# Kernel optimization log

Measured on AMD Instinct MI355X. Metric: run time of the kernel, lower is better.

## Reference

```python
import jax, jax.numpy as jnp
import numpy as np
import math

B, N, CS, CZ = 1, 512, 384, 128
GD = 16            # ipa_conf.c_hidden -> num 3D groups G
CH = GD * 3        # per-head hidden = 48
H = 8
PQ, PV = 8, 12
NF = 4             # num_frequencies
INF, EPS = 1e5, 1e-8
CZ4 = CZ // 4


def base_frequencies(num_freqs=NF, base=8.0, max_freq=1.0):
    fs = [min(base ** (-2 * i / num_freqs) * max_freq, max_freq) for i in range(num_freqs)]
    return jnp.asarray(fs, dtype=jnp.float32)


def hat(v):
    # v: [..., 3] -> skew-symmetric [..., 3, 3]
    x, y, z = v[..., 0], v[..., 1], v[..., 2]
    o = jnp.zeros_like(x)
    return jnp.stack([
        jnp.stack([o, -z, y], -1),
        jnp.stack([z, o, -x], -1),
        jnp.stack([-y, x, o], -1)], -2)


def setup_inputs() -> dict:
    key = jax.random.key(0)
    ks = jax.random.split(key, 24)
    std = 0.02
    hc = CH * H
    hpkv = H * (PQ + PV) * 3
    inp = {
        's': jax.random.normal(ks[0], (B, N, CS), jnp.float32),
        'z': jax.random.normal(ks[1], (B, N, N, CZ), jnp.float32),
        'rotvec': jax.random.normal(ks[2], (B, N, 3), jnp.float32),
        'mask': jnp.ones((B, N), jnp.float32),
        'wq': jax.random.normal(ks[3], (CS, hc), jnp.float32) * std,
        'bq': jnp.zeros((hc,), jnp.float32),
        'wkv': jax.random.normal(ks[4], (CS, 2 * hc), jnp.float32) * std,
        'bkv': jnp.zeros((2 * hc,), jnp.float32),
        'wkvp': jax.random.normal(ks[5], (CS, hpkv), jnp.float32) * std,
        'bkvp': jnp.zeros((hpkv,), jnp.float32),
        'wb': jax.random.normal(ks[6], (CZ, H), jnp.float32) * std,
        'bb': jnp.zeros((H,), jnp.float32),
        'wdz': jax.random.normal(ks[7], (CZ, CZ4), jnp.float32) * std,
        'bdz': jnp.zeros((CZ4,), jnp.float32),
        'wout': jax.random.normal(ks[8], (H * (CZ4 + CH + PV * 4), CS), jnp.float32) * std,
        'bout': jnp.zeros((CS,), jnp.float32),
        'log_freq_adj': jax.random.normal(ks[9], (NF,), jnp.float32) * std,
        'group_weights': jax.random.normal(ks[10], (GD,), jnp.float32) * std,
        'freq_weights': jnp.full((NF,), 1.0 / NF, jnp.float32),
    }
    return inp


def reference(s, z, rotvec, mask, wq, bq, wkv, bkv, wkvp, bkvp, wb, bb,
              wdz, bdz, wout, bout, log_freq_adj, group_weights, freq_weights):
    G = GD
    # projections
    q = (s @ wq + bq).reshape(B, N, H, CH)
    kv = (s @ wkv + bkv).reshape(B, N, H, 2 * CH)
    k, v = kv[..., :CH], kv[..., CH:]
    P = PQ + PV
    kvp = (s @ wkvp + bkvp).reshape(B, N, 3, H * P)      # torch split(...,3)+stack(-1)
    kvp = jnp.moveaxis(kvp, -2, -1).reshape(B, N, H, P, 3)
    v_pts = kvp[..., PQ:, :]                             # [B,N,H,PV,3]
    bias = z @ wb + bb                                   # [B,N,N,H]
    # RoPE-inspired multi-frequency Rodrigues rotations
    nrm = jnp.linalg.norm(rotvec, axis=-1, keepdims=True)
    angle = nrm + 1e-8                                   # [B,N,1]
    axis = rotvec / jnp.maximum(nrm, 1e-12)
    freqs = base_frequencies() * jnp.exp(log_freq_adj)   # [F]
    theta = angle * freqs                                # [B,N,F]
    K = hat(axis)                                        # [B,N,3,3]
    K2 = K @ K
    sin_t = jnp.sin(theta)[..., None, None]              # [B,N,F,1,1]
    cos_t = jnp.cos(theta)[..., None, None]
    I3 = jnp.eye(3, dtype=s.dtype)
    R = I3 + sin_t * K[:, :, None] + (1.0 - cos_t) * K2[:, :, None]  # [B,N,F,3,3]
    qg = q.reshape(B, N, H, G, 3)
    kg = k.reshape(B, N, H, G, 3)
    q_rot = jnp.einsum('bnfij,bnhgj->bnhgfi', R, qg)     # [B,N,H,G,F,3]
    k_rot = jnp.einsum('bnfij,bnhgj->bnhgfi', R, kg)
    # aggregation weights (sum over groups, softmax-weighted freqs)
    freq_w = jax.nn.softmax(freq_weights)
    group_w = jax.nn.softplus(group_weights) * math.sqrt(1.0 / G)
    qw = q_rot * freq_w[None, None, None, None, :, None] * group_w[None, None, None, :, None, None]
    scores = jnp.einsum('bihgfc,bjhgfc->bhij', qw, k_rot) / math.sqrt(3.0)
    a = scores + math.sqrt(1.0 / 3.0) * jnp.transpose(bias, (0, 3, 1, 2))
    sq_mask = INF * (mask[:, :, None] * mask[:, None, :] - 1.0)
    a = jax.nn.softmax(a + sq_mask[:, None], axis=-1)    # [B,H,N,N]
    # outputs
    o = jnp.einsum('bhij,bjhc->bihc', a, v).reshape(B, N, H * CH)
    o_pt = jnp.einsum('bhij,bjhpc->bihpc', a, v_pts)     # [B,N,H,PV,3]
    o_pt_norm = jnp.sqrt(jnp.sum(o_pt ** 2, -1) + EPS).reshape(B, N, H * PV)
    o_pt_flat = o_pt.reshape(B, N, H * PV, 3)
    pair_z = z @ wdz + bdz                               # [B,N,N,CZ4]
    o_pair = jnp.einsum('bhij,bijc->bihc', a, pair_z).reshape(B, N, H * CZ4)
    feats = jnp.concatenate([o, o_pt_flat[..., 0], o_pt_flat[..., 1],
                             o_pt_flat[..., 2], o_pt_norm, o_pair], axis=-1)
    return feats @ wout + bout                           # [B,N,CS]
```

## Files before the change

### kernel.cpp

```cpp
#include <hip/hip_runtime.h>
#include <math.h>


#define OFF_PROJ 0
#define SZ_PROJ (512*1632)
#define OFF_QW (OFF_PROJ + SZ_PROJ)
#define SZ_QW (8*512*192)
#define OFF_KST (OFF_QW + SZ_QW)
#define OFF_VCAT (OFF_KST + SZ_QW)
#define SZ_VCAT (512*768)
#define OFF_A (OFF_VCAT + SZ_VCAT)
#define SZ_A (8*512*512)
#define OFF_FEATS (OFF_A + SZ_A)
#define SZ_FEATS (512*1024)
#define OFF_PART (OFF_FEATS + SZ_FEATS)
#define SZ_PART (8*512*384)

__global__ __launch_bounds__(256) void proj_kernel(
    const float* __restrict__ s, const float* __restrict__ wq, const float* __restrict__ bq,
    const float* __restrict__ wkv, const float* __restrict__ bkv,
    const float* __restrict__ wkvp, const float* __restrict__ bkvp,
    float* __restrict__ proj)
{
  __shared__ float sT[384][34];
  int ct = blockIdx.x;
  int i0 = blockIdx.y * 32;
  int col0 = ct * 64;
  const float* W; const float* bias; int wld, wcol0;
  if (col0 < 384)       { W = wq;   bias = bq;   wld = 384; wcol0 = col0; }
  else if (col0 < 1152) { W = wkv;  bias = bkv;  wld = 768; wcol0 = col0 - 384; }
  else                  { W = wkvp; bias = bkvp; wld = 480; wcol0 = col0 - 1152; }
  int t = threadIdx.x;
  #pragma unroll
  for (int r = 0; r < 12; r++){
    int e = t + 256*r;
    int i = e & 31;
    int k4 = e >> 5;
    float4 v = *(const float4*)(s + (size_t)(i0 + i)*384 + k4*4);
    sT[k4*4+0][i] = v.x; sT[k4*4+1][i] = v.y; sT[k4*4+2][i] = v.z; sT[k4*4+3][i] = v.w;
  }
  __syncthreads();
  int cr = t & 15;
  int ipair = t >> 4;
  int ii = ipair * 2;
  int wc = wcol0 + cr*4;
  bool valid = (wc + 4 <= wld);
  int wcc = valid ? wc : (wld - 4);
  float acc[2][4];
  #pragma unroll
  for (int q = 0; q < 2; q++)
    #pragma unroll
    for (int p = 0; p < 4; p++) acc[q][p] = 0.f;
  #pragma unroll 4
  for (int k = 0; k < 384; k++){
    float2 a2 = *(const float2*)&sT[k][ii];
    float4 w4 = *(const float4*)(W + (size_t)k*wld + wcc);
    acc[0][0] = fmaf(a2.x, w4.x, acc[0][0]);
    acc[0][1] = fmaf(a2.x, w4.y, acc[0][1]);
    acc[0][2] = fmaf(a2.x, w4.z, acc[0][2]);
    acc[0][3] = fmaf(a2.x, w4.w, acc[0][3]);
    acc[1][0] = fmaf(a2.y, w4.x, acc[1][0]);
    acc[1][1] = fmaf(a2.y, w4.y, acc[1][1]);
    acc[1][2] = fmaf(a2.y, w4.z, acc[1][2]);
    acc[1][3] = fmaf(a2.y, w4.w, acc[1][3]);
  }
  if (valid){
    float4 bv = *(const float4*)(bias + wc);
    #pragma unroll
    for (int q = 0; q < 2; q++){
      int row = i0 + ii + q;
      float4 o;
      o.x = acc[q][0] + bv.x; o.y = acc[q][1] + bv.y;
      o.z = acc[q][2] + bv.z; o.w = acc[q][3] + bv.w;
      *(float4*)(proj + (size_t)row*1632 + col0 + cr*4) = o;
    }
  }
}

__global__ __launch_bounds__(128) void node_kernel(
    const float* __restrict__ proj, const float* __restrict__ rotvec,
    const float* __restrict__ lfa, const float* __restrict__ gwts, const float* __restrict__ fwts,
    float* __restrict__ Qw, float* __restrict__ Kst, float* __restrict__ Vcat)
{
  int i = blockIdx.x, t = threadIdx.x;
  const float* pr = proj + (size_t)i*1632;
  float rx = rotvec[i*3], ry = rotvec[i*3+1], rz = rotvec[i*3+2];
  float nrm = sqrtf(rx*rx + ry*ry + rz*rz);
  float angle = nrm + 1e-8f;
  float inv = 1.0f / fmaxf(nrm, 1e-12f);
  float ax = rx*inv, ay = ry*inv, az = rz*inv;
  float f0 = fwts[0], f1 = fwts[1], f2 = fwts[2], f3 = fwts[3];
  float mfw = fmaxf(fmaxf(f0,f1), fmaxf(f2,f3));
  float e0 = expf(f0-mfw), e1 = expf(f1-mfw), e2 = expf(f2-mfw), e3 = expf(f3-mfw);
  float esum = e0+e1+e2+e3;
  float fw[4] = {e0/esum, e1/esum, e2/esum, e3/esum};
  float fq[4] = { 1.0f*expf(lfa[0]), 0.35355339059327373f*expf(lfa[1]),
                  0.125f*expf(lfa[2]), 0.04419417382415922f*expf(lfa[3]) };
  int h = t >> 4, g = t & 15;
  float gw = log1pf(expf(gwts[g])) * 0.25f;
  float q0 = pr[h*48 + g*3 + 0], q1 = pr[h*48 + g*3 + 1], q2 = pr[h*48 + g*3 + 2];
  float k0 = pr[384 + h*96 + g*3 + 0], k1 = pr[384 + h*96 + g*3 + 1], k2 = pr[384 + h*96 + g*3 + 2];
  #pragma unroll
  for (int f = 0; f < 4; f++){
    float th = angle * fq[f];
    float sn = sinf(th), cs = cosf(th), omc = 1.0f - cs;
    float r00 = cs + omc*ax*ax,       r01 = omc*ax*ay - sn*az,  r02 = omc*ax*az + sn*ay;
    float r10 = omc*ay*ax + sn*az,    r11 = cs + omc*ay*ay,     r12 = omc*ay*az - sn*ax;
    float r20 = omc*az*ax - sn*ay,    r21 = omc*az*ay + sn*ax,  r22 = cs + omc*az*az;
    float qr0 = r00*q0 + r01*q1 + r02*q2;
    float qr1 = r10*q0 + r11*q1 + r12*q2;
    float qr2 = r20*q0 + r21*q1 + r22*q2;
    float kr0 = r00*k0 + r01*k1 + r02*k2;
    float kr1 = r10*k0 + r11*k1 + r12*k2;
    float kr2 = r20*k0 + r21*k1 + r22*k2;
    float sc = fw[f] * gw * 0.57735026918962576f;
    int base = (h*512 + i)*192 + (g*4 + f)*3;
    Qw[base+0] = qr0*sc; Qw[base+1] = qr1*sc; Qw[base+2] = qr2*sc;
    Kst[base+0] = kr0;   Kst[base+1] = kr1;   Kst[base+2] = kr2;
  }
  for (int c = t; c < 384; c += 128){
    int hh = c / 48, cc = c % 48;
    Vcat[(size_t)i*768 + hh*96 + cc] = pr[384 + hh*96 + 48 + cc];
  }
  for (int e = t; e < 288; e += 128){
    int hh = e / 36, r = e % 36;
    int p = r / 3, axv = r % 3;
    Vcat[(size_t)i*768 + hh*96 + 48 + p*3 + axv] = pr[1152 + axv*160 + hh*20 + 8 + p];
  }
}

__global__ __launch_bounds__(256) void zbias_kernel(
    const float* __restrict__ z, const float* __restrict__ wb, const float* __restrict__ bb,
    float* __restrict__ biasS)
{
  __shared__ float zs[8*1032];
  __shared__ float Wl[8*132];
  int i = blockIdx.y;
  int jt = blockIdx.x;
  int t = threadIdx.x;
  for (int r = 0; r < 4; r++){
    int e = t + 256*r;
    int ch = e & 7, k = e >> 3;
    Wl[ch*132 + k] = wb[k*8 + ch];
  }
  int cg = t >> 6, jg = t & 63;
  int ch0 = cg*2;
  float acc[2][4];
  #pragma unroll
  for (int c = 0; c < 2; c++)
    #pragma unroll
    for (int q = 0; q < 4; q++) acc[c][q] = 0.f;
  const float* zrow = z + ((size_t)i*512 + jt*256)*128;
  for (int kt = 0; kt < 4; kt++){
    __syncthreads();
    #pragma unroll
    for (int r = 0; r < 8; r++){
      int j = (t & 63) + 64*(r & 3);
      int kq = (t >> 6) + 4*(r >> 2);
      float4 v = *(const float4*)(zrow + (size_t)j*128 + kt*32 + kq*4);
      *(float4*)&zs[kq*1032 + j*4] = v;
    }
    __syncthreads();
    const float* wl0 = Wl + ch0*132 + kt*32;
    const float* wl1 = wl0 + 132;
    #pragma unroll
    for (int kq = 0; kq < 8; kq++){
      float4 w0 = *(const float4*)(wl0 + kq*4);
      float4 w1 = *(const float4*)(wl1 + kq*4);
      #pragma unroll
      for (int q = 0; q < 4; q++){
        float4 zv = *(const float4*)&zs[kq*1032 + (q*64 + jg)*4];
        acc[0][q] = fmaf(zv.x, w0.x, acc[0][q]);
        acc[0][q] = fmaf(zv.y, w0.y, acc[0][q]);
        acc[0][q] = fmaf(zv.z, w0.z, acc[0][q]);
        acc[0][q] = fmaf(zv.w, w0.w, acc[0][q]);
        acc[1][q] = fmaf(zv.x, w1.x, acc[1][q]);
        acc[1][q] = fmaf(zv.y, w1.y, acc[1][q]);
        acc[1][q] = fmaf(zv.z, w1.z, acc[1][q]);
        acc[1][q] = fmaf(zv.w, w1.w, acc[1][q]);
      }
    }
  }
  float b0 = bb[ch0], b1 = bb[ch0+1];
  #pragma unroll
  for (int q = 0; q < 4; q++){
    int j = jt*256 + q*64 + jg;
    biasS[(size_t)ch0*262144 + i*512 + j]     = 0.57735026918962576f * (acc[0][q] + b0);
    biasS[(size_t)(ch0+1)*262144 + i*512 + j] = 0.57735026918962576f * (acc[1][q] + b1);
  }
}

__global__ __launch_bounds__(256) void scores_kernel(
    const float* __restrict__ Qw, const float* __restrict__ Kst,
    const float* __restrict__ mask, float* A)
{
  __shared__ float Ks[4*2056];
  __shared__ float Qs[4*40];
  int i0 = blockIdx.x * 8;
  int h = blockIdx.y;
  int t = threadIdx.x;
  int ig = t >> 6, jl = t & 63;
  const float* Kb = Kst + (size_t)h*512*192;
  const float* Qb = Qw + (size_t)(h*512 + i0)*192;
  float acc[2][8];
  float mj[8];
  #pragma unroll
  for (int jt = 0; jt < 8; jt++) mj[jt] = mask[jt*64 + jl];
  #pragma unroll
  for (int q = 0; q < 2; q++){
    int i = i0 + ig*2 + q;
    float mi = mask[i];
    #pragma unroll
    for (int jt = 0; jt < 8; jt++){
      acc[q][jt] = A[((size_t)h*512 + i)*512 + jt*64 + jl] + 100000.0f*(mi*mj[jt] - 1.0f);
    }
  }
  for (int kc = 0; kc < 12; kc++){
    __syncthreads();
    {
      int k4 = t >> 6;
      #pragma unroll
      for (int r = 0; r < 8; r++){
        int j = (t & 63) + 64*r;
        float4 v = *(const float4*)(Kb + (size_t)j*192 + kc*16 + k4*4);
        *(float4*)&Ks[k4*2056 + j*4] = v;
      }
    }
    if (t < 32){
      int qi = t >> 2, k4 = t & 3;
      float4 v = *(const float4*)(Qb + (size_t)qi*192 + kc*16 + k4*4);
      *(float4*)&Qs[k4*40 + qi*4] = v;
    }
    __syncthreads();
    #pragma unroll
    for (int k4 = 0; k4 < 4; k4++){
      float4 qf[2];
      #pragma unroll
      for (int q = 0; q < 2; q++)
        qf[q] = *(const float4*)&Qs[k4*40 + (ig*2+q)*4];
      #pragma unroll
      for (int jt = 0; jt < 8; jt++){
        float4 kf = *(const float4*)&Ks[k4*2056 + (jt*64 + jl)*4];
        #pragma unroll
        for (int q = 0; q < 2; q++){
          acc[q][jt] = fmaf(qf[q].x, kf.x, acc[q][jt]);
          acc[q][jt] = fmaf(qf[q].y, kf.y, acc[q][jt]);
          acc[q][jt] = fmaf(qf[q].z, kf.z, acc[q][jt]);
          acc[q][jt] = fmaf(qf[q].w, kf.w, acc[q][jt]);
        }
      }
    }
  }
  #pragma unroll
  for (int q = 0; q < 2; q++){
    int i = i0 + ig*2 + q;
    float m = acc[q][0];
    #pragma unroll
    for (int jt = 1; jt < 8; jt++) m = fmaxf(m, acc[q][jt]);
    for (int off = 32; off > 0; off >>= 1) m = fmaxf(m, __shfl_xor(m, off));
    float ssum = 0.f;
    #pragma unroll
    for (int jt = 0; jt < 8; jt++){ acc[q][jt] = expf(acc[q][jt] - m); ssum += acc[q][jt]; }
    for (int off = 32; off > 0; off >>= 1) ssum += __shfl_xor(ssum, off);
    float invs = 1.0f / ssum;
    #pragma unroll
    for (int jt = 0; jt < 8; jt++){
      A[((size_t)h*512 + i)*512 + jt*64 + jl] = acc[q][jt] * invs;
    }
  }
}

__global__ __launch_bounds__(256) void yopair_kernel(
    const float* __restrict__ A, const float* __restrict__ z,
    const float* __restrict__ wdz, const float* __restrict__ bdz,
    float* __restrict__ feats)
{
  __shared__ float a_s[512*10];
  __shared__ float Y_s[8*132];
  int i = blockIdx.x;
  int t = threadIdx.x;
  #pragma unroll
  for (int r = 0; r < 4; r++){
    int idx = t + r*256;
    int h = idx >> 7, j4 = idx & 127;
    float4 v = *(const float4*)(A + ((size_t)h*512 + i)*512 + j4*4);
    a_s[(j4*4+0)*10 + h] = v.x;
    a_s[(j4*4+1)*10 + h] = v.y;
    a_s[(j4*4+2)*10 + h] = v.z;
    a_s[(j4*4+3)*10 + h] = v.w;
  }
  __syncthreads();
  int jh = t >> 7;
  int u = t & 127, hg = u >> 5, k4 = u & 31;
  int h0 = hg*2;
  const float* zb = z + ((size_t)i*512 + jh*256)*128 + k4*4;
  const float* ap = a_s + (jh*256)*10 + h0;
  float acc0[4], acc1[4];
  #pragma unroll
  for (int m = 0; m < 4; m++){ acc0[m] = 0.f; acc1[m] = 0.f; }
  #pragma unroll 8
  for (int j = 0; j < 256; j++){
    float2 a2 = *(const float2*)&ap[j*10];
    float4 zv = *(const float4*)(zb + (size_t)j*128);
    acc0[0] = fmaf(a2.x, zv.x, acc0[0]);
    acc0[1] = fmaf(a2.x, zv.y, acc0[1]);
    acc0[2] = fmaf(a2.x, zv.z, acc0[2]);
    acc0[3] = fmaf(a2.x, zv.w, acc0[3]);
    acc1[0] = fmaf(a2.y, zv.x, acc1[0]);
    acc1[1] = fmaf(a2.y, zv.y, acc1[1]);
    acc1[2] = fmaf(a2.y, zv.z, acc1[2]);
    acc1[3] = fmaf(a2.y, zv.w, acc1[3]);
  }
  if (jh == 0){
    *(float4*)&Y_s[h0*132 + k4*4]     = make_float4(acc0[0],acc0[1],acc0[2],acc0[3]);
    *(float4*)&Y_s[(h0+1)*132 + k4*4] = make_float4(acc1[0],acc1[1],acc1[2],acc1[3]);
  }
  __syncthreads();
  if (jh == 1){
    float4 p0 = *(const float4*)&Y_s[h0*132 + k4*4];
    float4 p1 = *(const float4*)&Y_s[(h0+1)*132 + k4*4];
    p0.x += acc0[0]; p0.y += acc0[1]; p0.z += acc0[2]; p0.w += acc0[3];
    p1.x += acc1[0]; p1.y += acc1[1]; p1.z += acc1[2]; p1.w += acc1[3];
    *(float4*)&Y_s[h0*132 + k4*4]     = p0;
    *(float4*)&Y_s[(h0+1)*132 + k4*4] = p1;
  }
  __syncthreads();
  int h = t >> 5, c = t & 31;
  float sacc = bdz[c];
  const float* Yr = Y_s + h*132;
  #pragma unroll 8
  for (int k = 0; k < 128; k++){
    sacc = fmaf(Yr[k], wdz[(size_t)k*32 + c], sacc);
  }
  feats[(size_t)i*1024 + 768 + h*32 + c] = sacc;
}

__global__ __launch_bounds__(256) void ovgemm_kernel(
    const float* __restrict__ A, const float* __restrict__ Vcat,
    float* __restrict__ feats)
{
  __shared__ float A_s[64*18];
  __shared__ float V_s[64*100];
  __shared__ float opt[16*40];
  int i0 = blockIdx.x * 16;
  int h = blockIdx.y;
  int t = threadIdx.x;
  int ip = t >> 5;
  int cg = t & 31;
  float acc[2][4];
  #pragma unroll
  for (int q = 0; q < 2; q++)
    #pragma unroll
    for (int m = 0; m < 4; m++) acc[q][m] = 0.f;
  for (int cb = 0; cb < 512; cb += 64){
    __syncthreads();
    {
      int ii = t >> 4, j4 = t & 15;
      float4 v = *(const float4*)(A + ((size_t)h*512 + i0 + ii)*512 + cb + j4*4);
      A_s[(j4*4+0)*18 + ii] = v.x;
      A_s[(j4*4+1)*18 + ii] = v.y;
      A_s[(j4*4+2)*18 + ii] = v.z;
      A_s[(j4*4+3)*18 + ii] = v.w;
    }
    #pragma unroll
    for (int r = 0; r < 6; r++){
      int idx = t + r*256;
      int j = idx / 24, cq = idx % 24;
      float4 v = *(const float4*)(Vcat + (size_t)(cb + j)*768 + h*96 + cq*4);
      *(float4*)&V_s[j*100 + cq*4] = v;
    }
    __syncthreads();
    #pragma unroll 4
    for (int k = 0; k < 64; k++){
      float2 a2 = *(const float2*)&A_s[k*18 + ip*2];
      float4 v4 = *(const float4*)&V_s[k*100 + cg*4];
      acc[0][0] = fmaf(a2.x, v4.x, acc[0][0]);
      acc[0][1] = fmaf(a2.x, v4.y, acc[0][1]);
      acc[0][2] = fmaf(a2.x, v4.z, acc[0][2]);
      acc[0][3] = fmaf(a2.x, v4.w, acc[0][3]);
      acc[1][0] = fmaf(a2.y, v4.x, acc[1][0]);
      acc[1][1] = fmaf(a2.y, v4.y, acc[1][1]);
      acc[1][2] = fmaf(a2.y, v4.z, acc[1][2]);
      acc[1][3] = fmaf(a2.y, v4.w, acc[1][3]);
    }
  }
  int c0 = cg*4;
  if (c0 < 48){
    #pragma unroll
    for (int q = 0; q < 2; q++){
      *(float4*)&feats[(size_t)(i0 + ip*2 + q)*1024 + h*48 + c0] =
        make_float4(acc[q][0], acc[q][1], acc[q][2], acc[q][3]);
    }
  } else if (c0 < 84){
    #pragma unroll
    for (int q = 0; q < 2; q++){
      #pragma unroll
      for (int m = 0; m < 4; m++){
        opt[(ip*2+q)*40 + (c0 - 48 + m)] = acc[q][m];
      }
    }
  }
  __syncthreads();
  if (t < 192){
    int il = t / 12, p = t % 12;
    float x = opt[il*40 + p*3], y = opt[il*40 + p*3 + 1], zz = opt[il*40 + p*3 + 2];
    float* fr = feats + (size_t)(i0 + il)*1024;
    fr[384 + h*12 + p] = x;
    fr[480 + h*12 + p] = y;
    fr[576 + h*12 + p] = zz;
    fr[672 + h*12 + p] = sqrtf(x*x + y*y + zz*zz + 1e-8f);
  }
}

__global__ __launch_bounds__(256) void outgemm_kernel(
    const float* __restrict__ feats, const float* __restrict__ wout,
    float* __restrict__ part)
{
  __shared__ float fA[32*68];
  __shared__ float fB[32*68];
  int ct = blockIdx.x;
  int it = blockIdx.y;
  int sk = blockIdx.z;
  int i0 = it*64, c0 = ct*64, k0 = sk*128;
  int t = threadIdx.x;
  int ir = t >> 4, cr = t & 15;
  float acc[4][4];
  #pragma unroll
  for (int q = 0; q < 4; q++)
    #pragma unroll
    for (int p = 0; p < 4; p++) acc[q][p] = 0.f;
  for (int kt = 0; kt < 128; kt += 32){
    __syncthreads();
    #pragma unroll
    for (int r = 0; r < 2; r++){
      int e = t + 256*r;
      int i = e & 63, kq = e >> 6;
      float4 v = *(const float4*)(feats + (size_t)(i0 + i)*1024 + k0 + kt + kq*4);
      fA[(kq*4+0)*68 + i] = v.x; fA[(kq*4+1)*68 + i] = v.y;
      fA[(kq*4+2)*68 + i] = v.z; fA[(kq*4+3)*68 + i] = v.w;
    }
    #pragma unroll
    for (int r = 0; r < 2; r++){
      int e = t + 256*r;
      int kk = e >> 4, c4 = e & 15;
      float4 v = *(const float4*)(wout + (size_t)(k0 + kt + kk)*384 + c0 + c4*4);
      *(float4*)&fB[kk*68 + c4*4] = v;
    }
    __syncthreads();
    #pragma unroll 8
    for (int k = 0; k < 32; k++){
      float4 a4 = *(const float4*)&fA[k*68 + ir*4];
      float4 b4 = *(const float4*)&fB[k*68 + cr*4];
      acc[0][0] = fmaf(a4.x, b4.x, acc[0][0]);
      acc[0][1] = fmaf(a4.x, b4.y, acc[0][1]);
      acc[0][2] = fmaf(a4.x, b4.z, acc[0][2]);
      acc[0][3] = fmaf(a4.x, b4.w, acc[0][3]);
      acc[1][0] = fmaf(a4.y, b4.x, acc[1][0]);
      acc[1][1] = fmaf(a4.y, b4.y, acc[1][1]);
      acc[1][2] = fmaf(a4.y, b4.z, acc[1][2]);
      acc[1][3] = fmaf(a4.y, b4.w, acc[1][3]);
      acc[2][0] = fmaf(a4.z, b4.x, acc[2][0]);
      acc[2][1] = fmaf(a4.z, b4.y, acc[2][1]);
      acc[2][2] = fmaf(a4.z, b4.z, acc[2][2]);
      acc[2][3] = fmaf(a4.z, b4.w, acc[2][3]);
      acc[3][0] = fmaf(a4.w, b4.x, acc[3][0]);
      acc[3][1] = fmaf(a4.w, b4.y, acc[3][1]);
      acc[3][2] = fmaf(a4.w, b4.z, acc[3][2]);
      acc[3][3] = fmaf(a4.w, b4.w, acc[3][3]);
    }
  }
  float* pb = part + ((size_t)sk*512 + i0)*384 + c0;
  #pragma unroll
  for (int q = 0; q < 4; q++){
    float4 o;
    o.x = acc[q][0]; o.y = acc[q][1]; o.z = acc[q][2]; o.w = acc[q][3];
    *(float4*)&pb[(size_t)(ir*4 + q)*384 + cr*4] = o;
  }
}

__global__ __launch_bounds__(256) void outreduce_kernel(
    const float* __restrict__ part, const float* __restrict__ bout,
    float* __restrict__ out)
{
  int e = blockIdx.x*256 + threadIdx.x;
  float4 acc = *(const float4*)(bout + (e % 96)*4);
  #pragma unroll
  for (int sk = 0; sk < 8; sk++){
    float4 p = *(const float4*)(part + (size_t)sk*196608 + (size_t)e*4);
    acc.x += p.x; acc.y += p.y; acc.z += p.z; acc.w += p.w;
  }
  *(float4*)(out + (size_t)e*4) = acc;
}

extern "C" void kernel_launch(void* const* d_in, const int* in_sizes, int n_in,
                              void* d_out, int out_size, void* d_ws, size_t ws_size,
                              hipStream_t stream)
{
  const float* s    = (const float*)d_in[0];
  const float* z    = (const float*)d_in[1];
  const float* rotv = (const float*)d_in[2];
  const float* mask = (const float*)d_in[3];
  const float* wq   = (const float*)d_in[4];
  const float* bq   = (const float*)d_in[5];
  const float* wkv  = (const float*)d_in[6];
  const float* bkv  = (const float*)d_in[7];
  const float* wkvp = (const float*)d_in[8];
  const float* bkvp = (const float*)d_in[9];
  const float* wb   = (const float*)d_in[10];
  const float* bb   = (const float*)d_in[11];
  const float* wdz  = (const float*)d_in[12];
  const float* bdz  = (const float*)d_in[13];
  const float* wout = (const float*)d_in[14];
  const float* bout = (const float*)d_in[15];
  const float* lfa  = (const float*)d_in[16];
  const float* gwts = (const float*)d_in[17];
  const float* fwts = (const float*)d_in[18];
  float* out = (float*)d_out;
  float* ws  = (float*)d_ws;

  float* proj  = ws + OFF_PROJ;
  float* Qw    = ws + OFF_QW;
  float* Kst   = ws + OFF_KST;
  float* Vcat  = ws + OFF_VCAT;
  float* A     = ws + OFF_A;
  float* feats = ws + OFF_FEATS;
  float* part  = ws + OFF_PART;

  proj_kernel     <<<dim3(26, 16), 256, 0, stream>>>(s, wq, bq, wkv, bkv, wkvp, bkvp, proj);
  node_kernel     <<<dim3(512),    128, 0, stream>>>(proj, rotv, lfa, gwts, fwts, Qw, Kst, Vcat);
  zbias_kernel    <<<dim3(2, 512), 256, 0, stream>>>(z, wb, bb, A);
  scores_kernel   <<<dim3(64, 8),  256, 0, stream>>>(Qw, Kst, mask, A);
  yopair_kernel   <<<dim3(512),    256, 0, stream>>>(A, z, wdz, bdz, feats);
  ovgemm_kernel   <<<dim3(32, 8),  256, 0, stream>>>(A, Vcat, feats);
  outgemm_kernel  <<<dim3(6, 8, 8),256, 0, stream>>>(feats, wout, part);
  outreduce_kernel<<<dim3(192),    256, 0, stream>>>(part, bout, out);
}
```

Before: 391.5 us.

## Fuse pair-z down-projection into z-bias pass, store bf16, read it in opair

The z-bias kernel now computes the 8 bias channels and the 32 down-projected pair channels in a single pass over z, writing pair_z as bf16 into a new workspace buffer. The opair kernel then reads this compact bf16 pair_z instead of rereading the full 128-channel fp32 z tensor. This removes a second full read of z (about 128 MB) in exchange for a 16 MB bf16 write and read, at some precision cost. Padded shared-memory strides are also added in the zbias and scores kernels to reduce LDS bank conflicts.

```diff
diff --git a/kernel.cpp b/kernel.cpp
--- a/kernel.cpp
+++ b/kernel.cpp
@@ -1,4 +1,5 @@
 #include <hip/hip_runtime.h>
+#include <hip/hip_bf16.h>
 #include <math.h>
 
 
@@ -11,7 +12,9 @@
 #define SZ_VCAT (512*768)
 #define OFF_A (OFF_VCAT + SZ_VCAT)
 #define SZ_A (8*512*512)
-#define OFF_FEATS (OFF_A + SZ_A)
+#define OFF_PZ (OFF_A + SZ_A)
+#define SZ_PZ (512*512*32/2)
+#define OFF_FEATS (OFF_PZ + SZ_PZ)
 #define SZ_FEATS (512*1024)
 #define OFF_PART (OFF_FEATS + SZ_FEATS)
 #define SZ_PART (8*512*384)
@@ -129,72 +132,84 @@
   }
 }
 
-__global__ __launch_bounds__(256) void zbias_kernel(
+#define ZPLANE 584
+__global__ __launch_bounds__(256) void zbias_pz_kernel(
     const float* __restrict__ z, const float* __restrict__ wb, const float* __restrict__ bb,
-    float* __restrict__ biasS)
-{
-  __shared__ float zs[8*1032];
-  __shared__ float Wl[8*132];
+    const float* __restrict__ wdz, const float* __restrict__ bdz,
+    float* __restrict__ biasS, ushort* __restrict__ PZ)
+{
+  __shared__ float zs[8*ZPLANE];
+  __shared__ float Wl[40*132];
   int i = blockIdx.y;
   int jt = blockIdx.x;
   int t = threadIdx.x;
-  for (int r = 0; r < 4; r++){
-    int e = t + 256*r;
-    int ch = e & 7, k = e >> 3;
-    Wl[ch*132 + k] = wb[k*8 + ch];
+  for (int e = t; e < 40*128; e += 256){
+    int ch = e % 40, k = e / 40;
+    Wl[ch*132 + k] = (ch < 8) ? wb[k*8 + ch] : wdz[k*32 + (ch - 8)];
   }
   int cg = t >> 6, jg = t & 63;
-  int ch0 = cg*2;
-  float acc[2][4];
-  #pragma unroll
-  for (int c = 0; c < 2; c++)
-    #pragma unroll
-    for (int q = 0; q < 4; q++) acc[c][q] = 0.f;
-  const float* zrow = z + ((size_t)i*512 + jt*256)*128;
+  int ch0 = cg*10;
+  float acc[10][2];
+  #pragma unroll
+  for (int cc = 0; cc < 10; cc++){ acc[cc][0] = 0.f; acc[cc][1] = 0.f; }
+  const float* zrow = z + ((size_t)i*512 + jt*128)*128;
+  int a0 = jg*4 + (jg>>3)*4;
+  int j1 = 64 + jg;
+  int a1 = j1*4 + (j1>>3)*4;
   for (int kt = 0; kt < 4; kt++){
     __syncthreads();
     #pragma unroll
-    for (int r = 0; r < 8; r++){
-      int j = (t & 63) + 64*(r & 3);
-      int kq = (t >> 6) + 4*(r >> 2);
+    for (int r = 0; r < 4; r++){
+      int idx = t + 256*r;
+      int kq = idx & 7, j = idx >> 3;
       float4 v = *(const float4*)(zrow + (size_t)j*128 + kt*32 + kq*4);
-      *(float4*)&zs[kq*1032 + j*4] = v;
-    }
-    __syncthreads();
-    const float* wl0 = Wl + ch0*132 + kt*32;
-    const float* wl1 = wl0 + 132;
+      *(float4*)&zs[kq*ZPLANE + j*4 + (j>>3)*4] = v;
+    }
+    __syncthreads();
     #pragma unroll
     for (int kq = 0; kq < 8; kq++){
-      float4 w0 = *(const float4*)(wl0 + kq*4);
-      float4 w1 = *(const float4*)(wl1 + kq*4);
+      float4 z0 = *(const float4*)&zs[kq*ZPLANE + a0];
+      float4 z1 = *(const float4*)&zs[kq*ZPLANE + a1];
       #pragma unroll
-      for (int q = 0; q < 4; q++){
-        float4 zv = *(const float4*)&zs[kq*1032 + (q*64 + jg)*4];
-        acc[0][q] = fmaf(zv.x, w0.x, acc[0][q]);
-        acc[0][q] = fmaf(zv.y, w0.y, acc[0][q]);
-        acc[0][q] = fmaf(zv.z, w0.z, acc[0][q]);
-        acc[0][q] = fmaf(zv.w, w0.w, acc[0][q]);
-        acc[1][q] = fmaf(zv.x, w1.x, acc[1][q]);
-        acc[1][q] = fmaf(zv.y, w1.y, acc[1][q]);
-        acc[1][q] = fmaf(zv.z, w1.z, acc[1][q]);
-        acc[1][q] = fmaf(zv.w, w1.w, acc[1][q]);
+      for (int cc = 0; cc < 10; cc++){
+        float4 w = *(const float4*)&Wl[(ch0+cc)*132 + kt*32 + kq*4];
+        acc[cc][0] = fmaf(z0.x, w.x, acc[cc][0]);
+        acc[cc][0] = fmaf(z0.y, w.y, acc[cc][0]);
+        acc[cc][0] = fmaf(z0.z, w.z, acc[cc][0]);
+        acc[cc][0] = fmaf(z0.w, w.w, acc[cc][0]);
+        acc[cc][1] = fmaf(z1.x, w.x, acc[cc][1]);
+        acc[cc][1] = fmaf(z1.y, w.y, acc[cc][1]);
+        acc[cc][1] = fmaf(z1.z, w.z, acc[cc][1]);
+        acc[cc][1] = fmaf(z1.w, w.w, acc[cc][1]);
       }
     }
   }
-  float b0 = bb[ch0], b1 = bb[ch0+1];
-  #pragma unroll
-  for (int q = 0; q < 4; q++){
-    int j = jt*256 + q*64 + jg;
-    biasS[(size_t)ch0*262144 + i*512 + j]     = 0.57735026918962576f * (acc[0][q] + b0);
-    biasS[(size_t)(ch0+1)*262144 + i*512 + j] = 0.57735026918962576f * (acc[1][q] + b1);
-  }
-}
-
+  #pragma unroll
+  for (int cc = 0; cc < 10; cc++){
+    int ch = ch0 + cc;
+    if (ch < 8){
+      float b = bb[ch];
+      float* bp = biasS + (size_t)ch*262144 + i*512 + jt*128 + jg;
+      bp[0]  = 0.57735026918962576f * (acc[cc][0] + b);
+      bp[64] = 0.57735026918962576f * (acc[cc][1] + b);
+    } else {
+      int c = ch - 8;
+      float b = bdz[c];
+      ushort* pp = PZ + ((size_t)i*32 + c)*512 + jt*128 + jg;
+      __hip_bfloat16 v0 = __float2bfloat16(acc[cc][0] + b);
+      __hip_bfloat16 v1 = __float2bfloat16(acc[cc][1] + b);
+      pp[0]  = *(ushort*)&v0;
+      pp[64] = *(ushort*)&v1;
+    }
+  }
+}
+
+#define KPLANE 2312
 __global__ __launch_bounds__(256) void scores_kernel(
     const float* __restrict__ Qw, const float* __restrict__ Kst,
     const float* __restrict__ mask, float* A)
 {
-  __shared__ float Ks[4*2056];
+  __shared__ float Ks[4*KPLANE];
   __shared__ float Qs[4*40];
   int i0 = blockIdx.x * 8;
   int h = blockIdx.y;
@@ -215,6 +230,12 @@
       acc[q][jt] = A[((size_t)h*512 + i)*512 + jt*64 + jl] + 100000.0f*(mi*mj[jt] - 1.0f);
     }
   }
+  int ja[8];
+  #pragma unroll
+  for (int jt = 0; jt < 8; jt++){
+    int j = jt*64 + jl;
+    ja[jt] = j*4 + (j>>3)*4;
+  }
   for (int kc = 0; kc < 12; kc++){
     __syncthreads();
     {
@@ -223,7 +244,7 @@
       for (int r = 0; r < 8; r++){
         int j = (t & 63) + 64*r;
         float4 v = *(const float4*)(Kb + (size_t)j*192 + kc*16 + k4*4);
-        *(float4*)&Ks[k4*2056 + j*4] = v;
+        *(float4*)&Ks[k4*KPLANE + j*4 + (j>>3)*4] = v;
       }
     }
     if (t < 32){
@@ -240,7 +261,7 @@
         qf[q] = *(const float4*)&Qs[k4*40 + (ig*2+q)*4];
       #pragma unroll
       for (int jt = 0; jt < 8; jt++){
-        float4 kf = *(const float4*)&Ks[k4*2056 + (jt*64 + jl)*4];
+        float4 kf = *(const float4*)&Ks[k4*KPLANE + ja[jt]];
         #pragma unroll
         for (int q = 0; q < 2; q++){
           acc[q][jt] = fmaf(qf[q].x, kf.x, acc[q][jt]);
@@ -270,13 +291,11 @@
   }
 }
 
-__global__ __launch_bounds__(256) void yopair_kernel(
-    const float* __restrict__ A, const float* __restrict__ z,
-    const float* __restrict__ wdz, const float* __restrict__ bdz,
+__global__ __launch_bounds__(256) void opair_kernel(
+    const float* __restrict__ A, const ushort* __restrict__ PZ,
     float* __restrict__ feats)
 {
   __shared__ float a_s[512*10];
-  __shared__ float Y_s[8*132];
   int i = blockIdx.x;
   int t = threadIdx.x;
   #pragma unroll
@@ -290,49 +309,23 @@
     a_s[(j4*4+3)*10 + h] = v.w;
   }
   __syncthreads();
-  int jh = t >> 7;
-  int u = t & 127, hg = u >> 5, k4 = u & 31;
-  int h0 = hg*2;
-  const float* zb = z + ((size_t)i*512 + jh*256)*128 + k4*4;
-  const float* ap = a_s + (jh*256)*10 + h0;
-  float acc0[4], acc1[4];
-  #pragma unroll
-  for (int m = 0; m < 4; m++){ acc0[m] = 0.f; acc1[m] = 0.f; }
+  int h = t >> 5, c = t & 31;
+  const ushort* pzb = PZ + ((size_t)i*32 + c)*512;
+  const float* ap = a_s + h;
+  float acc = 0.f;
   #pragma unroll 8
-  for (int j = 0; j < 256; j++){
-    float2 a2 = *(const float2*)&ap[j*10];
-    float4 zv = *(const float4*)(zb + (size_t)j*128);
-    acc0[0] = fmaf(a2.x, zv.x, acc0[0]);
-    acc0[1] = fmaf(a2.x, zv.y, acc0[1]);
-    acc0[2] = fmaf(a2.x, zv.z, acc0[2]);
-    acc0[3] = fmaf(a2.x, zv.w, acc0[3]);
-    acc1[0] = fmaf(a2.y, zv.x, acc1[0]);
-    acc1[1] = fmaf(a2.y, zv.y, acc1[1]);
-    acc1[2] = fmaf(a2.y, zv.z, acc1[2]);
-    acc1[3] = fmaf(a2.y, zv.w, acc1[3]);
-  }
-  if (jh == 0){
-    *(float4*)&Y_s[h0*132 + k4*4]     = make_float4(acc0[0],acc0[1],acc0[2],acc0[3]);
-    *(float4*)&Y_s[(h0+1)*132 + k4*4] = make_float4(acc1[0],acc1[1],acc1[2],acc1[3]);
-  }
-  __syncthreads();
-  if (jh == 1){
-    float4 p0 = *(const float4*)&Y_s[h0*132 + k4*4];
-    float4 p1 = *(const float4*)&Y_s[(h0+1)*132 + k4*4];
-    p0.x += acc0[0]; p0.y += acc0[1]; p0.z += acc0[2]; p0.w += acc0[3];
-    p1.x += acc1[0]; p1.y += acc1[1]; p1.z += acc1[2]; p1.w += acc1[3];
-    *(float4*)&Y_s[h0*132 + k4*4]     = p0;
-    *(float4*)&Y_s[(h0+1)*132 + k4*4] = p1;
-  }
-  __syncthreads();
-  int h = t >> 5, c = t & 31;
-  float sacc = bdz[c];
-  const float* Yr = Y_s + h*132;
-  #pragma unroll 8
-  for (int k = 0; k < 128; k++){
-    sacc = fmaf(Yr[k], wdz[(size_t)k*32 + c], sacc);
-  }
-  feats[(size_t)i*1024 + 768 + h*32 + c] = sacc;
+  for (int j4 = 0; j4 < 128; j4++){
+    ushort4 p4 = *(const ushort4*)(pzb + j4*4);
+    float z0 = __uint_as_float((unsigned)p4.x << 16);
+    float z1 = __uint_as_float((unsigned)p4.y << 16);
+    float z2 = __uint_as_float((unsigned)p4.z << 16);
+    float z3 = __uint_as_float((unsigned)p4.w << 16);
+    acc = fmaf(ap[(j4*4+0)*10], z0, acc);
+    acc = fmaf(ap[(j4*4+1)*10], z1, acc);
+    acc = fmaf(ap[(j4*4+2)*10], z2, acc);
+    acc = fmaf(ap[(j4*4+3)*10], z3, acc);
+  }
+  feats[(size_t)i*1024 + 768 + h*32 + c] = acc;
 }
 
 __global__ __launch_bounds__(256) void ovgemm_kernel(
@@ -523,14 +516,15 @@
   float* Kst   = ws + OFF_KST;
   float* Vcat  = ws + OFF_VCAT;
   float* A     = ws + OFF_A;
+  ushort* PZ   = (ushort*)(ws + OFF_PZ);
   float* feats = ws + OFF_FEATS;
   float* part  = ws + OFF_PART;
 
   proj_kernel     <<<dim3(26, 16), 256, 0, stream>>>(s, wq, bq, wkv, bkv, wkvp, bkvp, proj);
   node_kernel     <<<dim3(512),    128, 0, stream>>>(proj, rotv, lfa, gwts, fwts, Qw, Kst, Vcat);
-  zbias_kernel    <<<dim3(2, 512), 256, 0, stream>>>(z, wb, bb, A);
+  zbias_pz_kernel <<<dim3(4, 512), 256, 0, stream>>>(z, wb, bb, wdz, bdz, A, PZ);
   scores_kernel   <<<dim3(64, 8),  256, 0, stream>>>(Qw, Kst, mask, A);
-  yopair_kernel   <<<dim3(512),    256, 0, stream>>>(A, z, wdz, bdz, feats);
+  opair_kernel    <<<dim3(512),    256, 0, stream>>>(A, PZ, feats);
   ovgemm_kernel   <<<dim3(32, 8),  256, 0, stream>>>(A, Vcat, feats);
   outgemm_kernel  <<<dim3(6, 8, 8),256, 0, stream>>>(feats, wout, part);
   outreduce_kernel<<<dim3(192),    256, 0, stream>>>(part, bout, out);
```

After: 391.0 us. About the same (-0.1%).
